# Kernel optimization log

Hardware: AMD Instinct MI355X
Metric: run time of the kernel (lower is better)

## Reference

```python
import jax, jax.numpy as jnp
import numpy as np


def setup_inputs() -> dict:
    key = jax.random.key(0)
    x = jax.random.normal(key, (4, 3, 8192), dtype=jnp.float32)  # (B, 3, N)
    return {"x": x, "k": 30}


def reference(x, k):
    # x: (B, 3, N)
    x_t = jnp.swapaxes(x, 1, 2)  # (B, N, 3)
    xx = jnp.sum(x_t ** 2, axis=2, keepdims=True)  # (B, N, 1)
    # pairwise squared distances (B, N, N)
    pairwise = xx + jnp.swapaxes(xx, 1, 2) - 2.0 * jnp.matmul(x_t, x)
    # k smallest distances -> negate and take top_k
    _, idx = jax.lax.top_k(-pairwise, k)  # idx: (B, N, k)
    # gather neighbors: (B, N, k, 3)
    neighbors = jax.vmap(lambda pts, i: pts[i])(x_t, idx)
    centroid = jnp.mean(neighbors, axis=2, keepdims=True)  # (B, N, 1, 3)
    centered = neighbors - centroid  # (B, N, k, 3)
    # per-point 3x3 covariance
    cov = jnp.einsum('bnki,bnkj->bnij', centered, centered)  # (B, N, 3, 3)
    _, v = jnp.linalg.eigh(cov)  # eigenvalues ascending
    normals = v[..., :, 0]  # eigenvector of smallest eigenvalue, (B, N, 3)
    # orient normals toward viewpoint (origin): view_dir = -x_t
    dot = jnp.sum(-x_t * normals, axis=-1, keepdims=True)
    normals = jnp.where(dot < 0, -normals, normals)
    x_out = jnp.concatenate([x, jnp.swapaxes(normals, 1, 2)], axis=1)  # (B, 6, N)
    return x_out
```

## Files before the change

kernel.cpp:

```cpp
#include <hip/hip_runtime.h>
#include <math.h>

#define N_PTS   8192
#define KNN     30
#define CAPG    104
#define STR     105
#define GROUPS  8
#define BLOCK   128
#define NZ      64
#define NY      64
#define NBKT    (NZ * NY)
#define CLO     -4.0f
#define CSC     8.0f
#define BWID    0.125f
#define LAMBDA  48.0f


__device__ __forceinline__ int clampi(int v, int lo, int hi) {
    return v < lo ? lo : (v > hi ? hi : v);
}
__device__ __forceinline__ int bucket_of(float pz, float py) {
    int zb = clampi((int)floorf((pz - CLO) * CSC), 0, NZ - 1);
    int yb = clampi((int)floorf((py - CLO) * CSC), 0, NY - 1);
    return (zb << 6) | yb;
}

__global__ __launch_bounds__(1024) void histscan_kernel(const float* __restrict__ x,
                                                        int* __restrict__ bstart,
                                                        int* __restrict__ cur) {
    __shared__ int hist[NBKT];
    __shared__ int wtot[16];
    const int b = blockIdx.x, t = threadIdx.x;
    const int lane = t & 63, wid = t >> 6;
    const float* xb = x + (size_t)b * 3 * N_PTS;

    for (int k = t; k < NBKT; k += 1024) hist[k] = 0;
    __syncthreads();
    #pragma unroll
    for (int u = 0; u < 8; ++u) {
        int i = (u << 10) + t;
        float py = xb[N_PTS + i], pz = xb[2 * N_PTS + i];
        atomicAdd(&hist[bucket_of(pz, py)], 1);
    }
    __syncthreads();

    int base = t << 2;
    int l0 = hist[base], l1 = hist[base + 1], l2 = hist[base + 2], l3 = hist[base + 3];
    int s = l0 + l1 + l2 + l3;
    int sum = s;
    #pragma unroll
    for (int off = 1; off < 64; off <<= 1) {
        int v = __shfl_up(sum, off);
        if (lane >= off) sum += v;
    }
    if (lane == 63) wtot[wid] = sum;
    __syncthreads();
    int wbase = 0;
    #pragma unroll
    for (int k = 0; k < 16; ++k) wbase += (k < wid) ? wtot[k] : 0;
    int run = wbase + sum - s;
    int* bsb = bstart + b * (NBKT + 1);
    int* curb = cur + b * NBKT;
    bsb[base]     = run; curb[base]     = run; run += l0;
    bsb[base + 1] = run; curb[base + 1] = run; run += l1;
    bsb[base + 2] = run; curb[base + 2] = run; run += l2;
    bsb[base + 3] = run; curb[base + 3] = run;
    if (t == 1023) bsb[NBKT] = N_PTS;
}

__global__ __launch_bounds__(256) void scatter_kernel(const float* __restrict__ x,
                                                      float4* __restrict__ S,
                                                      int* __restrict__ O,
                                                      int* __restrict__ cur,
                                                      float* __restrict__ out) {
    int gid = blockIdx.x * 256 + threadIdx.x;
    int b = gid >> 13, i = gid & (N_PTS - 1);
    const float* xb = x + (size_t)b * 3 * N_PTS;
    float px = xb[i], py = xb[N_PTS + i], pz = xb[2 * N_PTS + i];
    float* ob = out + (size_t)b * 6 * N_PTS;
    ob[i]             = px;
    ob[N_PTS + i]     = py;
    ob[2 * N_PTS + i] = pz;
    float xx = __fadd_rn(__fadd_rn(__fmul_rn(px, px), __fmul_rn(py, py)),
                         __fmul_rn(pz, pz));
    int dst = atomicAdd(&cur[b * NBKT + bucket_of(pz, py)], 1);
    S[(b << 13) + dst] = make_float4(px, py, pz, xx);
    O[(b << 13) + dst] = i;
}

__global__ __launch_bounds__(BLOCK, 6) void knn_normal_kernel(const float4* __restrict__ S,
                                                              const int* __restrict__ O,
                                                              const int* __restrict__ bstart,
                                                              float* __restrict__ out) {
    __shared__ unsigned long long ldk[GROUPS * STR];

    const int t    = threadIdx.x;
    const int l16  = t & 15;
    const int g    = t >> 4;
    const int gsh  = (t & 63) & ~15;
    const int qblk = (blockIdx.x * 1031) & 4095;
    const int qid  = qblk * GROUPS + g;
    const int b    = qid >> 13;
    const int pos  = qid & (N_PTS - 1);
    const float4* __restrict__ P  = S + ((size_t)b << 13);
    const int*    __restrict__ Ob = O + ((size_t)b << 13);
    const int*    __restrict__ bs = bstart + b * (NBKT + 1);
    const float4 qp = P[pos];
    const int    oi = Ob[pos];

    unsigned long long* __restrict__ ldg = ldk + g * STR;

    const float c = fmaxf(sqrtf(qp.w), 1e-3f);
    float rlo = 0.05f, rhi = 6.0f;
    for (int it = 0; it < 14; ++it) {
        float r = 0.5f * (rlo + rhi);
        float slo = fmaxf(c - r, 0.0f);
        float h = (c + r - slo) * 0.125f;
        float f = 0.0f;
        if (l16 <= 8) {
            float sq = slo + h * (float)l16;
            float cs = c - sq;
            float hh = fmaxf(fminf((r * r - cs * cs) * (0.5f / c), 2.0f * sq), 0.0f);
            float w = (l16 == 0 || l16 == 8) ? 1.0f : ((l16 & 1) ? 4.0f : 2.0f);
            f = w * __expf(-0.5f * sq * sq) * sq * hh;
        }
        f += __shfl_xor(f, 1, 16); f += __shfl_xor(f, 2, 16);
        f += __shfl_xor(f, 4, 16); f += __shfl_xor(f, 8, 16);
        float lam = 1089.3f * f * h;
        if (lam < LAMBDA) rlo = r; else rhi = r;
    }
    float rad = rhi * 1.02f;
    float r2  = rad * rad;

    int  cnt = 0;
    bool active = true;

    for (;;) {
        if (active) {
            cnt = 0;
            float w  = __fmaf_rn(sqrtf(r2), 1.002f, 1e-3f);
            float w2 = w * w;
            int zlo = clampi((int)floorf((qp.z - w - CLO) * CSC), 0, NZ - 1);
            int zhi = clampi((int)floorf((qp.z + w - CLO) * CSC), 0, NZ - 1);
            for (int zb = zlo; zb <= zhi; ++zb) {
                float rz0 = CLO + (float)zb * BWID;
                float dz  = fmaxf(fmaxf(rz0 - qp.z, qp.z - (rz0 + BWID)), 0.0f);
                float yw  = sqrtf(fmaxf(w2 - dz * dz, 0.0f));
                int ylo = clampi((int)floorf((qp.y - yw - CLO) * CSC), 0, NY - 1);
                int yhi = clampi((int)floorf((qp.y + yw - CLO) * CSC), 0, NY - 1);
                int lo = bs[(zb << 6) + ylo];
                int hi = bs[(zb << 6) + yhi + 1];
                int smax = (hi - lo + 31) >> 5;
                for (int s = 0; s < smax; ++s) {
                    int j1  = lo + (s << 5) + l16;
                    int j2  = j1 + 16;
                    int jc1 = j1 < hi ? j1 : hi - 1;
                    int jc2 = j2 < hi ? j2 : hi - 1;
                    float4 p1 = P[jc1];
                    float4 p2 = P[jc2];
                    float mm1 = __fmaf_rn(qp.z, p1.z, __fmaf_rn(qp.y, p1.y, __fmul_rn(qp.x, p1.x)));
                    float d1  = __fsub_rn(__fadd_rn(qp.w, p1.w), __fmul_rn(2.0f, mm1));
                    float mm2 = __fmaf_rn(qp.z, p2.z, __fmaf_rn(qp.y, p2.y, __fmul_rn(qp.x, p2.x)));
                    float d2  = __fsub_rn(__fadd_rn(qp.w, p2.w), __fmul_rn(2.0f, mm2));
                    bool hit1 = (j1 < hi) && (d1 <= r2);
                    bool hit2 = (j2 < hi) && (d2 <= r2);
                    unsigned long long m1 = __ballot(hit1);
                    unsigned sub1 = (unsigned)((m1 >> gsh) & 0xFFFFull);
                    if (hit1) {
                        int slot = cnt + __popc(sub1 & ((1u << l16) - 1u));
                        if (slot < CAPG) {
                            unsigned u = __float_as_uint(d1);
                            u = (u & 0x80000000u) ? ~u : (u | 0x80000000u);
                            ldg[slot] = ((unsigned long long)u << 28) | (unsigned long long)jc1;
                        }
                    }
                    cnt += __popc(sub1);
                    unsigned long long m2 = __ballot(hit2);
                    unsigned sub2 = (unsigned)((m2 >> gsh) & 0xFFFFull);
                    if (hit2) {
                        int slot = cnt + __popc(sub2 & ((1u << l16) - 1u));
                        if (slot < CAPG) {
                            unsigned u = __float_as_uint(d2);
                            u = (u & 0x80000000u) ? ~u : (u | 0x80000000u);
                            ldg[slot] = ((unsigned long long)u << 28) | (unsigned long long)jc2;
                        }
                    }
                    cnt += __popc(sub2);
                }
            }
        }
        bool bad = active && (cnt < KNN || cnt > CAPG);
        if (__ballot(bad) == 0ULL) break;
        active = bad;
        if (active) r2 = (cnt < KNN) ? r2 * 1.6f : r2 * 0.82f;
    }

    unsigned long long mykey[7];
    #pragma unroll
    for (int m = 0; m < 7; ++m) mykey[m] = ~0ULL;
    {
        int nk = 0;
        for (int k = l16; k < cnt; k += 16) {
            unsigned long long key = ldg[k];
            int jc = (int)(key & 0x3FFFull);
            key = (key & ~0x0FFFFFFFull) | ((unsigned long long)Ob[jc] << 14)
                | (unsigned long long)jc;
            ldg[k] = key;
            mykey[nk++] = key;
        }
    }
    __syncthreads();

    int rank0 = 0, rank1 = 0, rank2 = 0, rank3 = 0, rank4 = 0, rank5 = 0, rank6 = 0;
    for (int u = 0; u < cnt; ++u) {
        unsigned long long ku = ldg[u];
        rank0 += (ku < mykey[0]) ? 1 : 0;
        rank1 += (ku < mykey[1]) ? 1 : 0;
        rank2 += (ku < mykey[2]) ? 1 : 0;
        rank3 += (ku < mykey[3]) ? 1 : 0;
        rank4 += (ku < mykey[4]) ? 1 : 0;
        rank5 += (ku < mykey[5]) ? 1 : 0;
        rank6 += (ku < mykey[6]) ? 1 : 0;
    }
    int rank[7] = { rank0, rank1, rank2, rank3, rank4, rank5, rank6 };

    const double qx = (double)qp.x, qy = (double)qp.y, qz = (double)qp.z;
    double sx = 0.0, sy = 0.0, sz = 0.0;
    double sxx = 0.0, sxy = 0.0, sxz = 0.0, syy = 0.0, syz = 0.0, szz = 0.0;

    #pragma unroll
    for (int m = 0; m < 7; ++m) {
        if (rank[m] < KNN) {
            float4 p = P[(int)(mykey[m] & 0x3FFFull)];
            double ax = (double)p.x - qx, ay = (double)p.y - qy, az = (double)p.z - qz;
            sx += ax; sy += ay; sz += az;
            sxx = fma(ax, ax, sxx); sxy = fma(ax, ay, sxy); sxz = fma(ax, az, sxz);
            syy = fma(ay, ay, syy); syz = fma(ay, az, syz); szz = fma(az, az, szz);
        }
    }

    #pragma unroll
    for (int off = 1; off < 16; off <<= 1) {
        sx  += __shfl_xor(sx,  off, 16); sy  += __shfl_xor(sy,  off, 16); sz  += __shfl_xor(sz,  off, 16);
        sxx += __shfl_xor(sxx, off, 16); sxy += __shfl_xor(sxy, off, 16); sxz += __shfl_xor(sxz, off, 16);
        syy += __shfl_xor(syy, off, 16); syz += __shfl_xor(syz, off, 16); szz += __shfl_xor(szz, off, 16);
    }

    if (l16 == 0) {
        const double kinv = 1.0 / (double)KNN;
        double m00 = sxx - sx * sx * kinv;
        double m11 = syy - sy * sy * kinv;
        double m22 = szz - sz * sz * kinv;
        double m01 = sxy - sx * sy * kinv;
        double m02 = sxz - sx * sz * kinv;
        double m12 = syz - sy * sz * kinv;

        double nx = 1.0, ny = 0.0, nz = 0.0;
        double q3 = (m00 + m11 + m22) / 3.0;
        double p1 = m01 * m01 + m02 * m02 + m12 * m12;
        double d00 = m00 - q3, d11 = m11 - q3, d22 = m22 - q3;
        double p2 = d00 * d00 + d11 * d11 + d22 * d22 + 2.0 * p1;
        if (p2 > 1e-280) {
            double pp = sqrt(p2 / 6.0);
            double ip = 1.0 / pp;
            double b00 = d00 * ip, b11 = d11 * ip, b22 = d22 * ip;
            double b01 = m01 * ip, b02 = m02 * ip, b12 = m12 * ip;
            double detB = b00 * (b11 * b22 - b12 * b12)
                        - b01 * (b01 * b22 - b12 * b02)
                        + b02 * (b01 * b12 - b11 * b02);
            double rr = 0.5 * detB;
            rr = rr < -1.0 ? -1.0 : (rr > 1.0 ? 1.0 : rr);
            double phi = acos(rr) / 3.0;
            double lam = q3 + 2.0 * pp * cos(phi + 2.0943951023931953);
            double a00 = m00 - lam, a11 = m11 - lam, a22 = m22 - lam;
            double v0x = m01 * m12 - m02 * a11, v0y = m02 * m01 - a00 * m12, v0z = a00 * a11 - m01 * m01;
            double v1x = m01 * a22 - m02 * m12, v1y = m02 * m02 - a00 * a22, v1z = a00 * m12 - m01 * m02;
            double v2x = a11 * a22 - m12 * m12, v2y = m12 * m02 - m01 * a22, v2z = m01 * m12 - a11 * m02;
            double n0 = v0x * v0x + v0y * v0y + v0z * v0z;
            double n1 = v1x * v1x + v1y * v1y + v1z * v1z;
            double n2 = v2x * v2x + v2y * v2y + v2z * v2z;
            double bx = v0x, by = v0y, bz = v0z, bn = n0;
            if (n1 > bn) { bx = v1x; by = v1y; bz = v1z; bn = n1; }
            if (n2 > bn) { bx = v2x; by = v2y; bz = v2z; bn = n2; }
            if (bn > 1e-280) {
                double inv = 1.0 / sqrt(bn);
                nx = bx * inv; ny = by * inv; nz = bz * inv;
            }
        }
        double dq = -(qx * nx + qy * ny + qz * nz);
        if (dq < 0.0) { nx = -nx; ny = -ny; nz = -nz; }

        float* ob = out + (size_t)b * 6 * N_PTS;
        ob[3 * N_PTS + oi] = (float)nx;
        ob[4 * N_PTS + oi] = (float)ny;
        ob[5 * N_PTS + oi] = (float)nz;
    }
}

extern "C" void kernel_launch(void* const* d_in, const int* in_sizes, int n_in,
                              void* d_out, int out_size, void* d_ws, size_t ws_size,
                              hipStream_t stream) {
    const float* x = (const float*)d_in[0];
    float* out = (float*)d_out;
    char* ws = (char*)d_ws;
    float4* S    = (float4*)(ws);
    int*    O    = (int*)(ws + 524288);
    int*    bsta = (int*)(ws + 655360);
    int*    cur  = (int*)(ws + 720912);

    histscan_kernel<<<dim3(4), dim3(1024), 0, stream>>>(x, bsta, cur);
    scatter_kernel<<<dim3(128), dim3(256), 0, stream>>>(x, S, O, cur, out);
    knn_normal_kernel<<<dim3(4096), dim3(BLOCK), 0, stream>>>(S, O, bsta, out);
}
```

Measured before the change: 164.7 us.

## Precompute per-point search radius in scatter kernel and shrink candidate capacity

The 14-step bisection that estimates each query's initial search radius moves from the kNN kernel, where it ran across 16-lane groups with shuffles, into the scatter kernel. There each thread computes it serially for its own point and stores r^2 in a new workspace array indexed by sorted position. The kNN kernel then loads that value. The candidate capacity also drops from 104 to 96, so each lane ranks 6 keys instead of 7, which cuts registers, LDS and the rank loop. The risks are more retry iterations when a query's candidate count exceeds the smaller cap, and more serial work in the small scatter launch.

```diff
diff --git a/kernel.cpp b/kernel.cpp
--- a/kernel.cpp
+++ b/kernel.cpp
@@ -3,8 +3,8 @@
 
 #define N_PTS   8192
 #define KNN     30
-#define CAPG    104
-#define STR     105
+#define CAPG    96
+#define STR     97
 #define GROUPS  8
 #define BLOCK   128
 #define NZ      64
@@ -71,6 +71,7 @@
 __global__ __launch_bounds__(256) void scatter_kernel(const float* __restrict__ x,
                                                       float4* __restrict__ S,
                                                       int* __restrict__ O,
+                                                      float* __restrict__ R,
                                                       int* __restrict__ cur,
                                                       float* __restrict__ out) {
     int gid = blockIdx.x * 256 + threadIdx.x;
@@ -86,11 +87,34 @@
     int dst = atomicAdd(&cur[b * NBKT + bucket_of(pz, py)], 1);
     S[(b << 13) + dst] = make_float4(px, py, pz, xx);
     O[(b << 13) + dst] = i;
+
+    const float c = fmaxf(sqrtf(xx), 1e-3f);
+    float rlo = 0.05f, rhi = 6.0f;
+    for (int it = 0; it < 14; ++it) {
+        float r = 0.5f * (rlo + rhi);
+        float slo = fmaxf(c - r, 0.0f), shi = c + r;
+        float h = (shi - slo) * 0.125f;
+        float acc = 0.0f;
+        #pragma unroll
+        for (int k = 0; k <= 8; ++k) {
+            float s  = slo + h * (float)k;
+            float cs = c - s;
+            float hh = fmaxf(fminf((r * r - cs * cs) * (0.5f / c), 2.0f * s), 0.0f);
+            float f = __expf(-0.5f * s * s) * s * hh;
+            float w = (k == 0 || k == 8) ? 1.0f : ((k & 1) ? 4.0f : 2.0f);
+            acc = fmaf(w, f, acc);
+        }
+        float lam = 1089.3f * acc * h;
+        if (lam < LAMBDA) rlo = r; else rhi = r;
+    }
+    float rad = rhi * 1.02f;
+    R[(b << 13) + dst] = rad * rad;
 }
 
 __global__ __launch_bounds__(BLOCK, 6) void knn_normal_kernel(const float4* __restrict__ S,
                                                               const int* __restrict__ O,
                                                               const int* __restrict__ bstart,
+                                                              const float* __restrict__ R,
                                                               float* __restrict__ out) {
     __shared__ unsigned long long ldk[GROUPS * STR];
 
@@ -110,28 +134,7 @@
 
     unsigned long long* __restrict__ ldg = ldk + g * STR;
 
-    const float c = fmaxf(sqrtf(qp.w), 1e-3f);
-    float rlo = 0.05f, rhi = 6.0f;
-    for (int it = 0; it < 14; ++it) {
-        float r = 0.5f * (rlo + rhi);
-        float slo = fmaxf(c - r, 0.0f);
-        float h = (c + r - slo) * 0.125f;
-        float f = 0.0f;
-        if (l16 <= 8) {
-            float sq = slo + h * (float)l16;
-            float cs = c - sq;
-            float hh = fmaxf(fminf((r * r - cs * cs) * (0.5f / c), 2.0f * sq), 0.0f);
-            float w = (l16 == 0 || l16 == 8) ? 1.0f : ((l16 & 1) ? 4.0f : 2.0f);
-            f = w * __expf(-0.5f * sq * sq) * sq * hh;
-        }
-        f += __shfl_xor(f, 1, 16); f += __shfl_xor(f, 2, 16);
-        f += __shfl_xor(f, 4, 16); f += __shfl_xor(f, 8, 16);
-        float lam = 1089.3f * f * h;
-        if (lam < LAMBDA) rlo = r; else rhi = r;
-    }
-    float rad = rhi * 1.02f;
-    float r2  = rad * rad;
-
+    float r2 = R[((size_t)b << 13) + pos];
     int  cnt = 0;
     bool active = true;
 
@@ -195,9 +198,9 @@
         if (active) r2 = (cnt < KNN) ? r2 * 1.6f : r2 * 0.82f;
     }
 
-    unsigned long long mykey[7];
-    #pragma unroll
-    for (int m = 0; m < 7; ++m) mykey[m] = ~0ULL;
+    unsigned long long mykey[6];
+    #pragma unroll
+    for (int m = 0; m < 6; ++m) mykey[m] = ~0ULL;
     {
         int nk = 0;
         for (int k = l16; k < cnt; k += 16) {
@@ -211,7 +214,7 @@
     }
     __syncthreads();
 
-    int rank0 = 0, rank1 = 0, rank2 = 0, rank3 = 0, rank4 = 0, rank5 = 0, rank6 = 0;
+    int rank0 = 0, rank1 = 0, rank2 = 0, rank3 = 0, rank4 = 0, rank5 = 0;
     for (int u = 0; u < cnt; ++u) {
         unsigned long long ku = ldg[u];
         rank0 += (ku < mykey[0]) ? 1 : 0;
@@ -220,16 +223,15 @@
         rank3 += (ku < mykey[3]) ? 1 : 0;
         rank4 += (ku < mykey[4]) ? 1 : 0;
         rank5 += (ku < mykey[5]) ? 1 : 0;
-        rank6 += (ku < mykey[6]) ? 1 : 0;
-    }
-    int rank[7] = { rank0, rank1, rank2, rank3, rank4, rank5, rank6 };
+    }
+    int rank[6] = { rank0, rank1, rank2, rank3, rank4, rank5 };
 
     const double qx = (double)qp.x, qy = (double)qp.y, qz = (double)qp.z;
     double sx = 0.0, sy = 0.0, sz = 0.0;
     double sxx = 0.0, sxy = 0.0, sxz = 0.0, syy = 0.0, syz = 0.0, szz = 0.0;
 
     #pragma unroll
-    for (int m = 0; m < 7; ++m) {
+    for (int m = 0; m < 6; ++m) {
         if (rank[m] < KNN) {
             float4 p = P[(int)(mykey[m] & 0x3FFFull)];
             double ax = (double)p.x - qx, ay = (double)p.y - qy, az = (double)p.z - qz;
@@ -307,8 +309,9 @@
     int*    O    = (int*)(ws + 524288);
     int*    bsta = (int*)(ws + 655360);
     int*    cur  = (int*)(ws + 720912);
+    float*  R    = (float*)(ws + 786448);
 
     histscan_kernel<<<dim3(4), dim3(1024), 0, stream>>>(x, bsta, cur);
-    scatter_kernel<<<dim3(128), dim3(256), 0, stream>>>(x, S, O, cur, out);
-    knn_normal_kernel<<<dim3(4096), dim3(BLOCK), 0, stream>>>(S, O, bsta, out);
-}
+    scatter_kernel<<<dim3(128), dim3(256), 0, stream>>>(x, S, O, R, cur, out);
+    knn_normal_kernel<<<dim3(4096), dim3(BLOCK), 0, stream>>>(S, O, bsta, R, out);
+}
```

After: 166.0 us. No clear change (+0.8%).
